# Optimization experiments

Hardware: AMD Instinct MI355X
Metric: run time of the kernel (lower is better)

## Reference

```python
import jax, jax.numpy as jnp
import numpy as np

D_MODEL = 1024
N_HEADS = 16
HEAD = D_MODEL // N_HEADS  # 64
D_FF = 4096
LN_EPS = 1e-5


def _layernorm(x, g, b):
    mu = jnp.mean(x, axis=-1, keepdims=True)
    var = jnp.mean(jnp.square(x - mu), axis=-1, keepdims=True)
    return (x - mu) * jax.lax.rsqrt(var + LN_EPS) * g + b


def _mha(q_in, k_in, v_in, Wq, Wk, Wv, bv, causal):
    # Wq/Wk/Wv: [H, d_model, head]; bv: [H, head] (value proj has bias, q/k do not)
    q = jnp.einsum('bsd,hde->bhse', q_in, Wq)
    k = jnp.einsum('btd,hde->bhte', k_in, Wk)
    v = jnp.einsum('btd,hde->bhte', v_in, Wv) + bv[None, :, None, :]
    scale = HEAD ** -0.5
    scores = jnp.einsum('bhse,bhte->bhst', q, k) * scale
    if causal:
        S, T = scores.shape[-2], scores.shape[-1]
        mask = jnp.tril(jnp.ones((S, T), dtype=bool))
        scores = jnp.where(mask, scores, -jnp.inf)
    p = jax.nn.softmax(scores, axis=-1)
    o = jnp.einsum('bhst,bhte->bhse', p, v)  # [B,H,S,head]
    B, H, S, E = o.shape
    return o.transpose(0, 2, 1, 3).reshape(B, S, H * E)  # concat heads in order


def setup_inputs() -> dict:
    key = jax.random.key(0)
    ks = jax.random.split(key, 20)
    B, S, T = 2, 2048, 2048
    sd = D_MODEL ** -0.5
    inp = {
        'input_tensor': jax.random.normal(ks[0], (B, S, D_MODEL), jnp.float32),
        'encoder_output': jax.random.normal(ks[1], (B, T, D_MODEL), jnp.float32),
        # masked self-attention params
        'Wq1': jax.random.normal(ks[2], (N_HEADS, D_MODEL, HEAD), jnp.float32) * sd,
        'Wk1': jax.random.normal(ks[3], (N_HEADS, D_MODEL, HEAD), jnp.float32) * sd,
        'Wv1': jax.random.normal(ks[4], (N_HEADS, D_MODEL, HEAD), jnp.float32) * sd,
        'bv1': jnp.zeros((N_HEADS, HEAD), jnp.float32),
        # cross-attention params
        'Wq2': jax.random.normal(ks[5], (N_HEADS, D_MODEL, HEAD), jnp.float32) * sd,
        'Wk2': jax.random.normal(ks[6], (N_HEADS, D_MODEL, HEAD), jnp.float32) * sd,
        'Wv2': jax.random.normal(ks[7], (N_HEADS, D_MODEL, HEAD), jnp.float32) * sd,
        'bv2': jnp.zeros((N_HEADS, HEAD), jnp.float32),
        # layernorms
        'g1': jnp.ones((D_MODEL,), jnp.float32), 'be1': jnp.zeros((D_MODEL,), jnp.float32),
        'g2': jnp.ones((D_MODEL,), jnp.float32), 'be2': jnp.zeros((D_MODEL,), jnp.float32),
        'g3': jnp.ones((D_MODEL,), jnp.float32), 'be3': jnp.zeros((D_MODEL,), jnp.float32),
        # FFN
        'Wf1': jax.random.normal(ks[8], (D_MODEL, D_FF), jnp.float32) * sd,
        'bf1': jnp.zeros((D_FF,), jnp.float32),
        'Wf2': jax.random.normal(ks[9], (D_FF, D_MODEL), jnp.float32) * (D_FF ** -0.5),
        'bf2': jnp.zeros((D_MODEL,), jnp.float32),
    }
    return inp


def reference(input_tensor, encoder_output, Wq1, Wk1, Wv1, bv1, Wq2, Wk2, Wv2, bv2,
              g1, be1, g2, be2, g3, be3, Wf1, bf1, Wf2, bf2):
    x = input_tensor
    # masked (causal) self-attention; dropout is identity in eval
    sa = _mha(x, x, x, Wq1, Wk1, Wv1, bv1, causal=True)
    x = _layernorm(sa + input_tensor, g1, be1)
    # cross-attention with encoder output (no mask)
    ca = _mha(x, encoder_output, encoder_output, Wq2, Wk2, Wv2, bv2, causal=False)
    x = _layernorm(x + ca, g2, be2)
    # FFN
    ffn = jax.nn.relu(x @ Wf1 + bf1) @ Wf2 + bf2
    x = _layernorm(x + ffn, g3, be3)
    return x
```

## Files before the change

kernel.cpp:

```cpp
#include <hip/hip_runtime.h>
#include <stdint.h>
#include <stddef.h>
#include <type_traits>

typedef __attribute__((ext_vector_type(8))) short short8;
typedef __attribute__((ext_vector_type(4))) short short4_t;
typedef __attribute__((ext_vector_type(4))) float float4_t;
typedef __attribute__((ext_vector_type(4))) unsigned uint4_t;

#define DEV static __device__ __forceinline__

#define QSCALE 0.18033688011112042f

DEV short f2bf(float f) {
  unsigned u = __builtin_bit_cast(unsigned, f);
  u = (u + 0x7FFFu + ((u >> 16) & 1u)) >> 16;
  return (short)(unsigned short)u;
}

DEV void load_lds16(const short* g, short* l) {
  __builtin_amdgcn_global_load_lds((const __attribute__((address_space(1))) void*)g,
                                   (__attribute__((address_space(3))) void*)l,
                                   16, 0, 0);
}

__global__ __launch_bounds__(256) void transpose_cvt(const float* __restrict__ src,
                                                     short* __restrict__ dst,
                                                     int R, int C) {
  __shared__ float t[64][65];
  src += (size_t)blockIdx.z * R * C;
  dst += (size_t)blockIdx.z * R * C;
  const int tid = threadIdx.x;
  const int r0 = blockIdx.y * 64, c0 = blockIdx.x * 64;
#pragma unroll
  for (int i = 0; i < 16; i++) {
    int r = i * 4 + (tid >> 6);
    t[r][tid & 63] = src[(size_t)(r0 + r) * C + c0 + (tid & 63)];
  }
  __syncthreads();
#pragma unroll
  for (int i = 0; i < 16; i++) {
    int c = i * 4 + (tid >> 6);
    dst[(size_t)(c0 + c) * R + r0 + (tid & 63)] = f2bf(t[tid & 63][c]);
  }
}

struct Repack6 {
  const float* src[6];
  short* dst[6];
};
__global__ __launch_bounds__(256) void transpose_cvt6(Repack6 a) {
  __shared__ float t[64][65];
  const int mat = blockIdx.z >> 4;
  const int head = blockIdx.z & 15;
  const float* src = a.src[mat] + (size_t)head * 1024 * 64;
  short* dst = a.dst[mat] + (size_t)head * 64 * 1024;
  const int tid = threadIdx.x;
  const int r0 = blockIdx.y * 64;
#pragma unroll
  for (int i = 0; i < 16; i++) {
    int r = i * 4 + (tid >> 6);
    t[r][tid & 63] = src[(size_t)(r0 + r) * 64 + (tid & 63)];
  }
  __syncthreads();
#pragma unroll
  for (int i = 0; i < 16; i++) {
    int c = i * 4 + (tid >> 6);
    dst[(size_t)c * 1024 + r0 + (tid & 63)] = f2bf(t[tid & 63][c]);
  }
}

__global__ __launch_bounds__(256) void cvt_bf16_2(const float* __restrict__ inA,
                                                  short* __restrict__ outA,
                                                  const float* __restrict__ inB,
                                                  short* __restrict__ outB, int n4) {
  int i = blockIdx.x * 256 + threadIdx.x;
  const float* in = blockIdx.z ? inB : inA;
  short* out = blockIdx.z ? outB : outA;
  if (i < n4) {
    float4_t v = ((const float4_t*)in)[i];
    short4_t o;
    o.x = f2bf(v.x); o.y = f2bf(v.y); o.z = f2bf(v.z); o.w = f2bf(v.w);
    ((short4_t*)out)[i] = o;
  }
}

struct GemmArgs {
  const short* A;
  const short* Bt;
  int M, N, K;
  float* outf;
  short* outb;
  short* Qo;
  short* Ko;
  short* Vt;
  const float* bias;
};

template <int MODE>
DEV void scatter1(const GemmArgs& args, int row, int col, float v) {
  if constexpr (MODE == 0) {
    int sel = col >> 10, cc = col & 1023;
    int h = cc >> 6, e = cc & 63;
    int b_ = row >> 11, s = row & 2047;
    if (sel == 0)
      args.Qo[(((size_t)(b_ * 16 + h)) * 2048 + s) * 64 + e] = f2bf(v * QSCALE);
    else if (sel == 1)
      args.Ko[(((size_t)(b_ * 16 + h)) * 2048 + s) * 64 + e] = f2bf(v);
    else {
      v += args.bias[cc];
      args.Vt[(((size_t)(b_ * 16 + h)) * 64 + e) * 2048 + s] = f2bf(v);
    }
  } else if constexpr (MODE == 1) {
    int h = col >> 6, e = col & 63;
    int b_ = row >> 11, s = row & 2047;
    args.Qo[(((size_t)(b_ * 16 + h)) * 2048 + s) * 64 + e] = f2bf(v * QSCALE);
  } else if constexpr (MODE == 2) {
    int sel = col >> 10, cc = col & 1023;
    int h = cc >> 6, e = cc & 63;
    int b_ = row >> 11, s = row & 2047;
    if (sel == 0)
      args.Ko[(((size_t)(b_ * 16 + h)) * 2048 + s) * 64 + e] = f2bf(v);
    else {
      v += args.bias[cc];
      args.Vt[(((size_t)(b_ * 16 + h)) * 64 + e) * 2048 + s] = f2bf(v);
    }
  } else if constexpr (MODE == 3) {
    v += args.bias[col];
    v = v > 0.f ? v : 0.f;
    args.outb[(size_t)row * args.N + col] = f2bf(v);
  } else {
    v += args.bias[col];
    args.outf[(size_t)row * args.N + col] = v;
  }
}

template <int MODE>
__global__ __launch_bounds__(256) void gemm_k(GemmArgs args) {
  constexpr int BM = 128, BK = 64;
  __shared__ short As[2][BM * BK];
  __shared__ short Bs[2][BM * BK];
  const int tid = threadIdx.x;
  const int lane = tid & 63;
  const int w = tid >> 6;
  const int wr = w >> 1, wc = w & 1;

  const int nwgx = gridDim.x;
  const int nxy = nwgx * gridDim.y;
  const int nwg = nxy * gridDim.z;
  const int orig = (blockIdx.z * gridDim.y + blockIdx.y) * nwgx + blockIdx.x;
  const int q8 = nwg >> 3;
  const int swz = (orig & 7) * q8 + (orig >> 3);
  const int zsl = swz / nxy;
  const int xy = swz % nxy;
  const int row0 = (xy / nwgx) * BM;
  const int col0 = (xy % nwgx) * BM;

  const int K = args.K;
  const int kLen = K / gridDim.z;
  const int kbase = zsl * kLen;
  const short* Ab = args.A + (size_t)row0 * K;
  const short* Bb = args.Bt + (size_t)col0 * K;
  float4_t acc[4][4] = {};
  const int r = lane & 15, kg = lane >> 4, rx = r & 7;

  auto stage = [&](int buf, int k0) {
#pragma unroll
    for (int i = 0; i < 4; i++) {
      int c = i * 256 + tid;
      int rw = c >> 3, sc = (c & 7) ^ (rw & 7);
      load_lds16(Ab + (size_t)rw * K + k0 + sc * 8, &As[buf][c * 8]);
    }
#pragma unroll
    for (int i = 0; i < 4; i++) {
      int c = i * 256 + tid;
      int rw = c >> 3, sc = (c & 7) ^ (rw & 7);
      load_lds16(Bb + (size_t)rw * K + k0 + sc * 8, &Bs[buf][c * 8]);
    }
  };

  stage(0, kbase);
  __syncthreads();
  int buf = 0;
  const int nk = kLen / BK;
  for (int t = 0; t < nk; t++) {
    if (t + 1 < nk) stage(buf ^ 1, kbase + (t + 1) * BK);
#pragma unroll
    for (int kk = 0; kk < BK; kk += 32) {
      const int ch = kk >> 3;
      short8 a[4], b[4];
#pragma unroll
      for (int m = 0; m < 4; m++)
        a[m] = *(const short8*)&As[buf][(wr * 64 + m * 16 + r) * BK + ((ch + kg) ^ rx) * 8];
#pragma unroll
      for (int n = 0; n < 4; n++)
        b[n] = *(const short8*)&Bs[buf][(wc * 64 + n * 16 + r) * BK + ((ch + kg) ^ rx) * 8];
#pragma unroll
      for (int m = 0; m < 4; m++)
#pragma unroll
        for (int n = 0; n < 4; n++)
          acc[m][n] = __builtin_amdgcn_mfma_f32_16x16x32_bf16(a[m], b[n], acc[m][n], 0, 0, 0);
    }
    __syncthreads();
    buf ^= 1;
  }

  float* dst5 = args.outf + (size_t)zsl * args.M * args.N;
#pragma unroll
  for (int m = 0; m < 4; m++)
#pragma unroll
    for (int n = 0; n < 4; n++)
#pragma unroll
      for (int j = 0; j < 4; j++) {
        int row = row0 + wr * 64 + m * 16 + kg * 4 + j;
        int col = col0 + wc * 64 + n * 16 + r;
        if constexpr (MODE == 5)
          dst5[(size_t)row * args.N + col] = acc[m][n][j];
        else
          scatter1<MODE>(args, row, col, acc[m][n][j]);
      }
}

template <int MODE>
__global__ __launch_bounds__(512, 2) void gemm256_k(GemmArgs args) {
  extern __shared__ short lds[];
  const int tid = threadIdx.x;
  const int lane = tid & 63;
  const int w = tid >> 6;
  const int wr = w >> 2, wc = w & 3;

  const int nwgx = gridDim.x;
  const int nwg = nwgx * gridDim.y;
  const int orig = blockIdx.y * nwgx + blockIdx.x;
  const int q8 = nwg >> 3;
  const int swz = (orig & 7) * q8 + (orig >> 3);
  const int row0 = (swz / nwgx) * 256;
  const int col0 = (swz % nwgx) * 256;

  const int K = args.K;
  const short* Ab = args.A + (size_t)row0 * K;
  const short* Bb = args.Bt + (size_t)col0 * K;
  const int r = lane & 15, kg = lane >> 4, rx = r & 7;
  float4_t acc[8][4] = {};

  auto stage = [&](int buf, int k0) {
    short* Ad = lds + buf * 16384;
    short* Bd = lds + 32768 + buf * 16384;
#pragma unroll
    for (int i = 0; i < 4; i++) {
      int c = i * 512 + tid;
      int rw = c >> 3, sc = (c & 7) ^ (rw & 7);
      load_lds16(Ab + (size_t)rw * K + k0 + sc * 8, Ad + c * 8);
    }
#pragma unroll
    for (int i = 0; i < 4; i++) {
      int c = i * 512 + tid;
      int rw = c >> 3, sc = (c & 7) ^ (rw & 7);
      load_lds16(Bb + (size_t)rw * K + k0 + sc * 8, Bd + c * 8);
    }
  };

  stage(0, 0);
  __syncthreads();
  int buf = 0;
  const int nk = K / 64;
  for (int t = 0; t < nk; t++) {
    if (t + 1 < nk) stage(buf ^ 1, (t + 1) * 64);
    const short* Ar = lds + buf * 16384;
    const short* Br = lds + 32768 + buf * 16384;
#pragma unroll
    for (int kk = 0; kk < 64; kk += 32) {
      const int ch = kk >> 3;
      short8 a[8], b[4];
#pragma unroll
      for (int m = 0; m < 8; m++)
        a[m] = *(const short8*)&Ar[(wr * 128 + m * 16 + r) * 64 + ((ch + kg) ^ rx) * 8];
#pragma unroll
      for (int n = 0; n < 4; n++)
        b[n] = *(const short8*)&Br[(wc * 64 + n * 16 + r) * 64 + ((ch + kg) ^ rx) * 8];
#pragma unroll
      for (int m = 0; m < 8; m++)
#pragma unroll
        for (int n = 0; n < 4; n++)
          acc[m][n] = __builtin_amdgcn_mfma_f32_16x16x32_bf16(a[m], b[n], acc[m][n], 0, 0, 0);
    }
    __syncthreads();
    buf ^= 1;
  }

#pragma unroll
  for (int m = 0; m < 8; m++)
#pragma unroll
    for (int n = 0; n < 4; n++)
#pragma unroll
      for (int j = 0; j < 4; j++)
        scatter1<MODE>(args, row0 + wr * 128 + m * 16 + kg * 4 + j,
                       col0 + wc * 64 + n * 16 + r, acc[m][n][j]);
}

template <bool CAUSAL>
__global__ __launch_bounds__(256) void attn_k(const short* __restrict__ Q,
                                              const short* __restrict__ Kq,
                                              const short* __restrict__ Vt,
                                              float* __restrict__ Out) {
  __shared__ short kst[2][64 * 64];
  __shared__ short vst[2][64 * 64];
  __shared__ unsigned p_lds[4][16 * 32];
  const int tid = threadIdx.x;
  const int lane = tid & 63;
  const int w = tid >> 6;
  const int bh = blockIdx.y;
  const int b_ = bh >> 4, h = bh & 15;
  const int qt = (blockIdx.x + blockIdx.y) & (gridDim.x - 1);
  const int q0 = qt * 64 + w * 16;
  const int r = lane & 15, kg = lane >> 4;
  const int rx = r & 7;
  const size_t base = (size_t)bh * 2048 * 64;
  const short* Qb = Q + base;
  const short* Kb = Kq + base;
  const short* Vb = Vt + base;

  short8 q[2];
#pragma unroll
  for (int half = 0; half < 2; half++)
    q[half] = *(const short8*)&Qb[(size_t)(q0 + r) * 64 + half * 32 + kg * 8];

  float4_t o[4] = {};
  float lp = 0.f;

  const int NT = CAUSAL ? qt + 1 : 32;
  const float4_t zero4 = {0.f, 0.f, 0.f, 0.f};

  const int c0 = tid, c1 = tid + 256;
  const int row0s = c0 >> 3, cc0 = (c0 & 7) ^ (row0s & 7);
  const int row1s = c1 >> 3, cc1 = (c1 & 7) ^ (row1s & 7);

  auto stage = [&](int buf, int kt) {
    const short* ktk = Kb + (size_t)kt * 64 * 64;
    const short* ktv = Vb + (size_t)kt * 64;
    load_lds16(ktk + row0s * 64 + cc0 * 8, &kst[buf][c0 * 8]);
    load_lds16(ktk + row1s * 64 + cc1 * 8, &kst[buf][c1 * 8]);
    load_lds16(ktv + (size_t)row0s * 2048 + cc0 * 8, &vst[buf][c0 * 8]);
    load_lds16(ktv + (size_t)row1s * 2048 + cc1 * 8, &vst[buf][c1 * 8]);
  };

  auto body = [&](auto BUFC, int kt) {
    constexpr int BUF = decltype(BUFC)::value;
    short8 kb[4][2];
#pragma unroll
    for (int grp = 0; grp < 4; grp++)
#pragma unroll
      for (int half = 0; half < 2; half++)
        kb[grp][half] = *(const short8*)&kst[BUF][(grp * 16 + r) * 64 + ((half * 4 + kg) ^ rx) * 8];

    float4_t sc[4];
    __builtin_amdgcn_s_setprio(1);
#pragma unroll
    for (int grp = 0; grp < 4; grp++) {
      float4_t t0 = __builtin_amdgcn_mfma_f32_16x16x32_bf16(kb[grp][0], q[0], zero4, 0, 0, 0);
      sc[grp] = __builtin_amdgcn_mfma_f32_16x16x32_bf16(kb[grp][1], q[1], t0, 0, 0, 0);
    }
    __builtin_amdgcn_s_setprio(0);

    float s[16];
#pragma unroll
    for (int grp = 0; grp < 4; grp++)
#pragma unroll
      for (int j = 0; j < 4; j++) s[grp * 4 + j] = sc[grp][j];

    if (CAUSAL && kt == NT - 1) {
      const int qrow = q0 + r;
#pragma unroll
      for (int grp = 0; grp < 4; grp++)
#pragma unroll
        for (int j = 0; j < 4; j++)
          if (kt * 64 + grp * 16 + kg * 4 + j > qrow) s[grp * 4 + j] = -1e30f;
    }

    float p[16];
    float ps = 0.f;
#pragma unroll
    for (int i = 0; i < 16; i++) {
      p[i] = __builtin_amdgcn_exp2f(s[i]);
      ps += p[i];
    }
    lp += ps;

    unsigned* p32 = &p_lds[w][0];
#pragma unroll
    for (int grp = 0; grp < 4; grp++) {
      unsigned pk01, pk23;
      asm("v_cvt_pk_bf16_f32 %0, %1, %2" : "=v"(pk01) : "v"(p[grp * 4 + 0]), "v"(p[grp * 4 + 1]));
      asm("v_cvt_pk_bf16_f32 %0, %1, %2" : "=v"(pk23) : "v"(p[grp * 4 + 2]), "v"(p[grp * 4 + 3]));
      int idx = r * 32 + ((2 * grp + (kg >> 1)) ^ rx) * 4 + (kg & 1) * 2;
      p32[idx] = pk01;
      p32[idx + 1] = pk23;
    }
    __builtin_amdgcn_sched_barrier(0);

    short8 pa[2];
#pragma unroll
    for (int half = 0; half < 2; half++) {
      const int db = r * 32 + ((half * 4 + kg) ^ rx) * 4;
      uint4_t t;
      t.x = p32[db + 0];
      t.y = p32[db + 1];
      t.z = p32[db + 2];
      t.w = p32[db + 3];
      pa[half] = __builtin_bit_cast(short8, t);
    }

    __builtin_amdgcn_s_setprio(1);
#pragma unroll
    for (int n = 0; n < 4; n++) {
      short8 v0 = *(const short8*)&vst[BUF][(n * 16 + r) * 64 + ((0 * 4 + kg) ^ rx) * 8];
      short8 v1 = *(const short8*)&vst[BUF][(n * 16 + r) * 64 + ((1 * 4 + kg) ^ rx) * 8];
      o[n] = __builtin_amdgcn_mfma_f32_16x16x32_bf16(v0, pa[0], o[n], 0, 0, 0);
      o[n] = __builtin_amdgcn_mfma_f32_16x16x32_bf16(v1, pa[1], o[n], 0, 0, 0);
    }
    __builtin_amdgcn_s_setprio(0);
  };

  stage(0, 0);
  __syncthreads();

  for (int kt = 0; kt < NT; kt += 2) {
    if (kt + 1 < NT) stage(1, kt + 1);
    body(std::integral_constant<int, 0>{}, kt);
    __syncthreads();
    if (kt + 1 >= NT) break;
    if (kt + 2 < NT) stage(0, kt + 2);
    body(std::integral_constant<int, 1>{}, kt + 1);
    __syncthreads();
  }

  lp += __shfl_xor(lp, 16);
  lp += __shfl_xor(lp, 32);
  const float inv = 1.0f / lp;
  float* orow = Out + ((size_t)b_ * 2048 + q0 + r) * 1024 + h * 64;
#pragma unroll
  for (int n = 0; n < 4; n++)
#pragma unroll
    for (int j = 0; j < 4; j++)
      orow[n * 16 + kg * 4 + j] = o[n][j] * inv;
}

__global__ __launch_bounds__(256) void add_ln_k(const float* __restrict__ X,
                                                const float* __restrict__ Y,
                                                const float* __restrict__ g,
                                                const float* __restrict__ be,
                                                float* __restrict__ outf,
                                                short* __restrict__ outb) {
  __shared__ float red[8];
  const int row = blockIdx.x;
  const int t = threadIdx.x;
  const int lane = t & 63, w = t >> 6;
  float4_t v = ((const float4_t*)(X + (size_t)row * 1024))[t];
  float4_t u = ((const float4_t*)(Y + (size_t)row * 1024))[t];
  v.x += u.x; v.y += u.y; v.z += u.z; v.w += u.w;
  float s = v.x + v.y + v.z + v.w;
#pragma unroll
  for (int off = 32; off >= 1; off >>= 1) s += __shfl_xor(s, off);
  if (lane == 0) red[w] = s;
  __syncthreads();
  float mean = (red[0] + red[1] + red[2] + red[3]) * (1.f / 1024.f);
  float dx = v.x - mean, dy = v.y - mean, dz = v.z - mean, dw = v.w - mean;
  float q2 = dx * dx + dy * dy + dz * dz + dw * dw;
#pragma unroll
  for (int off = 32; off >= 1; off >>= 1) q2 += __shfl_xor(q2, off);
  if (lane == 0) red[4 + w] = q2;
  __syncthreads();
  float var = (red[4] + red[5] + red[6] + red[7]) * (1.f / 1024.f);
  float rs = rsqrtf(var + 1e-5f);
  float4_t gg = ((const float4_t*)g)[t];
  float4_t bb = ((const float4_t*)be)[t];
  float4_t o;
  o.x = dx * rs * gg.x + bb.x;
  o.y = dy * rs * gg.y + bb.y;
  o.z = dz * rs * gg.z + bb.z;
  o.w = dw * rs * gg.w + bb.w;
  ((float4_t*)(outf + (size_t)row * 1024))[t] = o;
  if (outb != nullptr) {
    short4_t ob;
    ob.x = f2bf(o.x); ob.y = f2bf(o.y); ob.z = f2bf(o.z); ob.w = f2bf(o.w);
    ((short4_t*)(outb + (size_t)row * 1024))[t] = ob;
  }
}

__global__ __launch_bounds__(256) void add_ln2_k(const float* __restrict__ X,
                                                 const float* __restrict__ P0,
                                                 const float* __restrict__ P1,
                                                 const float* __restrict__ bias,
                                                 const float* __restrict__ g,
                                                 const float* __restrict__ be,
                                                 float* __restrict__ outf) {
  __shared__ float red[8];
  const int row = blockIdx.x;
  const int t = threadIdx.x;
  const int lane = t & 63, w = t >> 6;
  float4_t v = ((const float4_t*)(X + (size_t)row * 1024))[t];
  float4_t u0 = ((const float4_t*)(P0 + (size_t)row * 1024))[t];
  float4_t u1 = ((const float4_t*)(P1 + (size_t)row * 1024))[t];
  float4_t bi = ((const float4_t*)bias)[t];
  v.x += u0.x + u1.x + bi.x;
  v.y += u0.y + u1.y + bi.y;
  v.z += u0.z + u1.z + bi.z;
  v.w += u0.w + u1.w + bi.w;
  float s = v.x + v.y + v.z + v.w;
#pragma unroll
  for (int off = 32; off >= 1; off >>= 1) s += __shfl_xor(s, off);
  if (lane == 0) red[w] = s;
  __syncthreads();
  float mean = (red[0] + red[1] + red[2] + red[3]) * (1.f / 1024.f);
  float dx = v.x - mean, dy = v.y - mean, dz = v.z - mean, dw = v.w - mean;
  float q2 = dx * dx + dy * dy + dz * dz + dw * dw;
#pragma unroll
  for (int off = 32; off >= 1; off >>= 1) q2 += __shfl_xor(q2, off);
  if (lane == 0) red[4 + w] = q2;
  __syncthreads();
  float var = (red[4] + red[5] + red[6] + red[7]) * (1.f / 1024.f);
  float rs = rsqrtf(var + 1e-5f);
  float4_t gg = ((const float4_t*)g)[t];
  float4_t bb = ((const float4_t*)be)[t];
  float4_t o;
  o.x = dx * rs * gg.x + bb.x;
  o.y = dy * rs * gg.y + bb.y;
  o.z = dz * rs * gg.z + bb.z;
  o.w = dw * rs * gg.w + bb.w;
  ((float4_t*)(outf + (size_t)row * 1024))[t] = o;
}

extern "C" void kernel_launch(void* const* d_in, const int* in_sizes, int n_in,
                              void* d_out, int out_size, void* d_ws, size_t ws_size,
                              hipStream_t stream) {
  (void)in_sizes; (void)n_in; (void)out_size; (void)ws_size;
  const float* x_in = (const float*)d_in[0];
  const float* enc  = (const float*)d_in[1];
  const float* Wq1  = (const float*)d_in[2];
  const float* Wk1  = (const float*)d_in[3];
  const float* Wv1  = (const float*)d_in[4];
  const float* bv1  = (const float*)d_in[5];
  const float* Wq2  = (const float*)d_in[6];
  const float* Wk2  = (const float*)d_in[7];
  const float* Wv2  = (const float*)d_in[8];
  const float* bv2  = (const float*)d_in[9];
  const float* g1   = (const float*)d_in[10];
  const float* be1  = (const float*)d_in[11];
  const float* g2   = (const float*)d_in[12];
  const float* be2  = (const float*)d_in[13];
  const float* g3   = (const float*)d_in[14];
  const float* be3  = (const float*)d_in[15];
  const float* Wf1  = (const float*)d_in[16];
  const float* bf1  = (const float*)d_in[17];
  const float* Wf2  = (const float*)d_in[18];
  const float* bf2  = (const float*)d_in[19];
  float* out = (float*)d_out;

  (void)hipFuncSetAttribute((const void*)gemm256_k<0>,
                            hipFuncAttributeMaxDynamicSharedMemorySize, 131072);
  (void)hipFuncSetAttribute((const void*)gemm256_k<3>,
                            hipFuncAttributeMaxDynamicSharedMemorySize, 131072);

  char* ws = (char*)d_ws;
  size_t off = 0;
  auto alloc = [&](size_t bytes) -> void* {
    void* p = ws + off;
    off += (bytes + 255) & ~(size_t)255;
    return p;
  };
  short* wqkv1t = (short*)alloc((size_t)3072 * 1024 * 2);
  short* wq2t   = (short*)alloc((size_t)1024 * 1024 * 2);
  short* wkv2t  = (short*)alloc((size_t)2048 * 1024 * 2);
  short* wf1t   = (short*)alloc((size_t)4096 * 1024 * 2);
  short* wf2t   = (short*)alloc((size_t)1024 * 4096 * 2);
  short* act_bf = (short*)alloc((size_t)4096 * 1024 * 2);
  short* enc_bf = (short*)alloc((size_t)4096 * 1024 * 2);
  short* Qb     = (short*)alloc((size_t)4096 * 1024 * 2);
  short* Kb     = (short*)alloc((size_t)4096 * 1024 * 2);
  short* Vtb    = (short*)alloc((size_t)4096 * 1024 * 2);
  float* tmp_f  = (float*)alloc((size_t)4096 * 1024 * 4);
  float* xbuf   = (float*)alloc((size_t)4096 * 1024 * 4);
  short* h_bf   = (short*)alloc((size_t)4096 * 4096 * 2);
  float* pbuf   = (float*)alloc((size_t)2 * 4096 * 1024 * 4);

  dim3 blk(256);
  dim3 blk5(512);
  Repack6 rp;
  rp.src[0] = Wq1; rp.dst[0] = wqkv1t;
  rp.src[1] = Wk1; rp.dst[1] = wqkv1t + 1024 * 1024;
  rp.src[2] = Wv1; rp.dst[2] = wqkv1t + 2 * 1024 * 1024;
  rp.src[3] = Wq2; rp.dst[3] = wq2t;
  rp.src[4] = Wk2; rp.dst[4] = wkv2t;
  rp.src[5] = Wv2; rp.dst[5] = wkv2t + 1024 * 1024;
  transpose_cvt6<<<dim3(1, 16, 96), blk, 0, stream>>>(rp);
  transpose_cvt<<<dim3(64, 16, 1), blk, 0, stream>>>(Wf1, wf1t, 1024, 4096);
  transpose_cvt<<<dim3(16, 64, 1), blk, 0, stream>>>(Wf2, wf2t, 4096, 1024);
  cvt_bf16_2<<<dim3(4096, 1, 2), blk, 0, stream>>>(x_in, act_bf, enc, enc_bf, 1048576);

  GemmArgs ga;
  ga.A = act_bf; ga.Bt = wqkv1t; ga.M = 4096; ga.N = 3072; ga.K = 1024;
  ga.outf = nullptr; ga.outb = nullptr; ga.Qo = Qb; ga.Ko = Kb; ga.Vt = Vtb; ga.bias = bv1;
  gemm256_k<0><<<dim3(12, 16), blk5, 131072, stream>>>(ga);
  attn_k<true><<<dim3(32, 32), blk, 0, stream>>>(Qb, Kb, Vtb, tmp_f);
  add_ln_k<<<4096, blk, 0, stream>>>(tmp_f, x_in, g1, be1, xbuf, act_bf);

  ga.A = act_bf; ga.Bt = wq2t; ga.M = 4096; ga.N = 1024; ga.K = 1024;
  ga.Qo = Qb; ga.Ko = nullptr; ga.Vt = nullptr; ga.bias = nullptr;
  gemm_k<1><<<dim3(8, 32), blk, 0, stream>>>(ga);
  ga.A = enc_bf; ga.Bt = wkv2t; ga.M = 4096; ga.N = 2048; ga.K = 1024;
  ga.Qo = nullptr; ga.Ko = Kb; ga.Vt = Vtb; ga.bias = bv2;
  gemm_k<2><<<dim3(16, 32), blk, 0, stream>>>(ga);
  attn_k<false><<<dim3(32, 32), blk, 0, stream>>>(Qb, Kb, Vtb, tmp_f);
  add_ln_k<<<4096, blk, 0, stream>>>(xbuf, tmp_f, g2, be2, xbuf, act_bf);

  ga.A = act_bf; ga.Bt = wf1t; ga.M = 4096; ga.N = 4096; ga.K = 1024;
  ga.outb = h_bf; ga.bias = bf1; ga.Qo = nullptr; ga.Ko = nullptr; ga.Vt = nullptr;
  gemm256_k<3><<<dim3(16, 16), blk5, 131072, stream>>>(ga);
  ga.A = h_bf; ga.Bt = wf2t; ga.M = 4096; ga.N = 1024; ga.K = 4096;
  ga.outf = pbuf; ga.outb = nullptr; ga.bias = nullptr;
  gemm_k<5><<<dim3(8, 32, 2), blk, 0, stream>>>(ga);
  add_ln2_k<<<4096, blk, 0, stream>>>(xbuf, pbuf, pbuf + (size_t)4096 * 1024,
                                      bf2, g3, be3, out);
}
```

Before: 343.5 us.

## Process 32 query rows per wave in attention to reuse K/V tiles

Each wave in the attention kernel now handles two 16-row query groups, so a block covers 128 query rows and the grid is halved. Every K/V tile loaded into LDS and read into registers is reused by twice as many queries, which cuts K/V global traffic and LDS reads per unit of work. The causal tile order is also mirrored across the batch-head halves to balance the triangular workload. The cost is higher register and LDS use per wave, which may lower occupancy, and fewer blocks in flight.

```diff
diff --git a/kernel.cpp b/kernel.cpp
--- a/kernel.cpp
+++ b/kernel.cpp
@@ -305,14 +305,15 @@
                                               float* __restrict__ Out) {
   __shared__ short kst[2][64 * 64];
   __shared__ short vst[2][64 * 64];
-  __shared__ unsigned p_lds[4][16 * 32];
+  __shared__ unsigned p_lds[4][32 * 32];
   const int tid = threadIdx.x;
   const int lane = tid & 63;
   const int w = tid >> 6;
   const int bh = blockIdx.y;
   const int b_ = bh >> 4, h = bh & 15;
-  const int qt = (blockIdx.x + blockIdx.y) & (gridDim.x - 1);
-  const int q0 = qt * 64 + w * 16;
+  const int qb = (blockIdx.x + blockIdx.y) & 15;
+  const int qt = (blockIdx.y & 16) ? (15 - qb) : qb;
+  const int q0w = qt * 128 + w * 32;
   const int r = lane & 15, kg = lane >> 4;
   const int rx = r & 7;
   const size_t base = (size_t)bh * 2048 * 64;
@@ -320,15 +321,17 @@
   const short* Kb = Kq + base;
   const short* Vb = Vt + base;
 
-  short8 q[2];
-#pragma unroll
-  for (int half = 0; half < 2; half++)
-    q[half] = *(const short8*)&Qb[(size_t)(q0 + r) * 64 + half * 32 + kg * 8];
-
-  float4_t o[4] = {};
-  float lp = 0.f;
-
-  const int NT = CAUSAL ? qt + 1 : 32;
+  short8 q[2][2];
+#pragma unroll
+  for (int qg = 0; qg < 2; qg++)
+#pragma unroll
+    for (int half = 0; half < 2; half++)
+      q[qg][half] = *(const short8*)&Qb[(size_t)(q0w + qg * 16 + r) * 64 + half * 32 + kg * 8];
+
+  float4_t o[2][4] = {};
+  float lp[2] = {0.f, 0.f};
+
+  const int NT = CAUSAL ? 2 * qt + 2 : 32;
   const float4_t zero4 = {0.f, 0.f, 0.f, 0.f};
 
   const int c0 = tid, c1 = tid + 256;
@@ -353,70 +356,78 @@
       for (int half = 0; half < 2; half++)
         kb[grp][half] = *(const short8*)&kst[BUF][(grp * 16 + r) * 64 + ((half * 4 + kg) ^ rx) * 8];
 
-    float4_t sc[4];
-    __builtin_amdgcn_s_setprio(1);
-#pragma unroll
-    for (int grp = 0; grp < 4; grp++) {
-      float4_t t0 = __builtin_amdgcn_mfma_f32_16x16x32_bf16(kb[grp][0], q[0], zero4, 0, 0, 0);
-      sc[grp] = __builtin_amdgcn_mfma_f32_16x16x32_bf16(kb[grp][1], q[1], t0, 0, 0, 0);
-    }
-    __builtin_amdgcn_s_setprio(0);
-
-    float s[16];
-#pragma unroll
-    for (int grp = 0; grp < 4; grp++)
-#pragma unroll
-      for (int j = 0; j < 4; j++) s[grp * 4 + j] = sc[grp][j];
-
-    if (CAUSAL && kt == NT - 1) {
-      const int qrow = q0 + r;
+    unsigned* p32 = &p_lds[w][0];
+#pragma unroll
+    for (int qg = 0; qg < 2; qg++) {
+      float4_t sc[4];
+      __builtin_amdgcn_s_setprio(1);
+#pragma unroll
+      for (int grp = 0; grp < 4; grp++) {
+        float4_t t0 = __builtin_amdgcn_mfma_f32_16x16x32_bf16(kb[grp][0], q[qg][0], zero4, 0, 0, 0);
+        sc[grp] = __builtin_amdgcn_mfma_f32_16x16x32_bf16(kb[grp][1], q[qg][1], t0, 0, 0, 0);
+      }
+      __builtin_amdgcn_s_setprio(0);
+
+      float s[16];
 #pragma unroll
       for (int grp = 0; grp < 4; grp++)
 #pragma unroll
-        for (int j = 0; j < 4; j++)
-          if (kt * 64 + grp * 16 + kg * 4 + j > qrow) s[grp * 4 + j] = -1e30f;
-    }
-
-    float p[16];
-    float ps = 0.f;
-#pragma unroll
-    for (int i = 0; i < 16; i++) {
-      p[i] = __builtin_amdgcn_exp2f(s[i]);
-      ps += p[i];
-    }
-    lp += ps;
-
-    unsigned* p32 = &p_lds[w][0];
-#pragma unroll
-    for (int grp = 0; grp < 4; grp++) {
-      unsigned pk01, pk23;
-      asm("v_cvt_pk_bf16_f32 %0, %1, %2" : "=v"(pk01) : "v"(p[grp * 4 + 0]), "v"(p[grp * 4 + 1]));
-      asm("v_cvt_pk_bf16_f32 %0, %1, %2" : "=v"(pk23) : "v"(p[grp * 4 + 2]), "v"(p[grp * 4 + 3]));
-      int idx = r * 32 + ((2 * grp + (kg >> 1)) ^ rx) * 4 + (kg & 1) * 2;
-      p32[idx] = pk01;
-      p32[idx + 1] = pk23;
+        for (int j = 0; j < 4; j++) s[grp * 4 + j] = sc[grp][j];
+
+      if (CAUSAL && kt >= 2 * qt) {
+        const int qrow = q0w + qg * 16 + r;
+#pragma unroll
+        for (int grp = 0; grp < 4; grp++)
+#pragma unroll
+          for (int j = 0; j < 4; j++)
+            if (kt * 64 + grp * 16 + kg * 4 + j > qrow) s[grp * 4 + j] = -1e30f;
+      }
+
+      float p[16];
+      float ps = 0.f;
+#pragma unroll
+      for (int i = 0; i < 16; i++) {
+        p[i] = __builtin_amdgcn_exp2f(s[i]);
+        ps += p[i];
+      }
+      lp[qg] += ps;
+
+#pragma unroll
+      for (int grp = 0; grp < 4; grp++) {
+        unsigned pk01, pk23;
+        asm("v_cvt_pk_bf16_f32 %0, %1, %2" : "=v"(pk01) : "v"(p[grp * 4 + 0]), "v"(p[grp * 4 + 1]));
+        asm("v_cvt_pk_bf16_f32 %0, %1, %2" : "=v"(pk23) : "v"(p[grp * 4 + 2]), "v"(p[grp * 4 + 3]));
+        int idx = (qg * 16 + r) * 32 + ((2 * grp + (kg >> 1)) ^ rx) * 4 + (kg & 1) * 2;
+        p32[idx] = pk01;
+        p32[idx + 1] = pk23;
+      }
     }
     __builtin_amdgcn_sched_barrier(0);
 
-    short8 pa[2];
-#pragma unroll
-    for (int half = 0; half < 2; half++) {
-      const int db = r * 32 + ((half * 4 + kg) ^ rx) * 4;
-      uint4_t t;
-      t.x = p32[db + 0];
-      t.y = p32[db + 1];
-      t.z = p32[db + 2];
-      t.w = p32[db + 3];
-      pa[half] = __builtin_bit_cast(short8, t);
-    }
+    short8 pa[2][2];
+#pragma unroll
+    for (int qg = 0; qg < 2; qg++)
+#pragma unroll
+      for (int half = 0; half < 2; half++) {
+        const int db = (qg * 16 + r) * 32 + ((half * 4 + kg) ^ rx) * 4;
+        uint4_t t;
+        t.x = p32[db + 0];
+        t.y = p32[db + 1];
+        t.z = p32[db + 2];
+        t.w = p32[db + 3];
+        pa[qg][half] = __builtin_bit_cast(short8, t);
+      }
 
     __builtin_amdgcn_s_setprio(1);
 #pragma unroll
     for (int n = 0; n < 4; n++) {
       short8 v0 = *(const short8*)&vst[BUF][(n * 16 + r) * 64 + ((0 * 4 + kg) ^ rx) * 8];
       short8 v1 = *(const short8*)&vst[BUF][(n * 16 + r) * 64 + ((1 * 4 + kg) ^ rx) * 8];
-      o[n] = __builtin_amdgcn_mfma_f32_16x16x32_bf16(v0, pa[0], o[n], 0, 0, 0);
-      o[n] = __builtin_amdgcn_mfma_f32_16x16x32_bf16(v1, pa[1], o[n], 0, 0, 0);
+#pragma unroll
+      for (int qg = 0; qg < 2; qg++) {
+        o[qg][n] = __builtin_amdgcn_mfma_f32_16x16x32_bf16(v0, pa[qg][0], o[qg][n], 0, 0, 0);
+        o[qg][n] = __builtin_amdgcn_mfma_f32_16x16x32_bf16(v1, pa[qg][1], o[qg][n], 0, 0, 0);
+      }
     }
     __builtin_amdgcn_s_setprio(0);
   };
@@ -434,15 +445,19 @@
     __syncthreads();
   }
 
-  lp += __shfl_xor(lp, 16);
-  lp += __shfl_xor(lp, 32);
-  const float inv = 1.0f / lp;
-  float* orow = Out + ((size_t)b_ * 2048 + q0 + r) * 1024 + h * 64;
-#pragma unroll
-  for (int n = 0; n < 4; n++)
-#pragma unroll
-    for (int j = 0; j < 4; j++)
-      orow[n * 16 + kg * 4 + j] = o[n][j] * inv;
+#pragma unroll
+  for (int qg = 0; qg < 2; qg++) {
+    float l = lp[qg];
+    l += __shfl_xor(l, 16);
+    l += __shfl_xor(l, 32);
+    const float inv = 1.0f / l;
+    float* orow = Out + ((size_t)b_ * 2048 + q0w + qg * 16 + r) * 1024 + h * 64;
+#pragma unroll
+    for (int n = 0; n < 4; n++)
+#pragma unroll
+      for (int j = 0; j < 4; j++)
+        orow[n * 16 + kg * 4 + j] = o[qg][n][j] * inv;
+  }
 }
 
 __global__ __launch_bounds__(256) void add_ln_k(const float* __restrict__ X,
@@ -601,7 +616,7 @@
   ga.A = act_bf; ga.Bt = wqkv1t; ga.M = 4096; ga.N = 3072; ga.K = 1024;
   ga.outf = nullptr; ga.outb = nullptr; ga.Qo = Qb; ga.Ko = Kb; ga.Vt = Vtb; ga.bias = bv1;
   gemm256_k<0><<<dim3(12, 16), blk5, 131072, stream>>>(ga);
-  attn_k<true><<<dim3(32, 32), blk, 0, stream>>>(Qb, Kb, Vtb, tmp_f);
+  attn_k<true><<<dim3(16, 32), blk, 0, stream>>>(Qb, Kb, Vtb, tmp_f);
   add_ln_k<<<4096, blk, 0, stream>>>(tmp_f, x_in, g1, be1, xbuf, act_bf);
 
   ga.A = act_bf; ga.Bt = wq2t; ga.M = 4096; ga.N = 1024; ga.K = 1024;
@@ -610,7 +625,7 @@
   ga.A = enc_bf; ga.Bt = wkv2t; ga.M = 4096; ga.N = 2048; ga.K = 1024;
   ga.Qo = nullptr; ga.Ko = Kb; ga.Vt = Vtb; ga.bias = bv2;
   gemm_k<2><<<dim3(16, 32), blk, 0, stream>>>(ga);
-  attn_k<false><<<dim3(32, 32), blk, 0, stream>>>(Qb, Kb, Vtb, tmp_f);
+  attn_k<false><<<dim3(16, 32), blk, 0, stream>>>(Qb, Kb, Vtb, tmp_f);
   add_ln_k<<<4096, blk, 0, stream>>>(xbuf, tmp_f, g2, be2, xbuf, act_bf);
 
   ga.A = act_bf; ga.Bt = wf1t; ga.M = 4096; ga.N = 4096; ga.K = 1024;
```

After: 338.5 us (median of 2 runs). About the same (-1.5%).
